# Performance work log

Measured on AMD Instinct MI355X. Metric: run time of the kernel, lower is better.

The kernel has to match this reference:

```python
import jax, jax.numpy as jnp
import numpy as np
import math

N = 8_000_000
EPS = 0.0


def setup_inputs() -> dict:
    key = jax.random.key(0)
    x = jax.random.normal(key, (N, 3), dtype=jnp.float32)
    return {"x": x}


def _normalize(x, eps):
    # faithful to _safe_norm: sn = sum(x^2) + eps^2; eps==0 -> guard zero vectors
    sn = jnp.sum(x * x, axis=-1, keepdims=True) + eps * eps
    if eps == 0.0:
        sn_safe = jnp.where(sn == 0.0, 1.0, sn)
        inv = jnp.where(sn == 0.0, 0.0, jax.lax.rsqrt(sn_safe))
        return x * inv
    return x * jax.lax.rsqrt(sn)


def _sh_l0to3(u):
    # u: (..., 3) unit vectors; real spherical harmonics, e3nn/cuEquivariance
    # "component" normalization (|Y^l(u)|^2 = 2l+1 on the unit sphere).
    vx, vy, vz = u[..., 0], u[..., 1], u[..., 2]
    x2, y2, z2 = vx * vx, vy * vy, vz * vz
    x2z2 = x2 + z2

    sh0 = jnp.ones_like(vx)[..., None]                      # (..., 1)

    sh1 = math.sqrt(3.0) * u                                # (..., 3)

    s15 = math.sqrt(15.0)
    sh2_0 = s15 * vx * vz
    sh2_1 = s15 * vx * vy
    sh2_2 = math.sqrt(5.0) * (y2 - 0.5 * x2z2)
    sh2_3 = s15 * vy * vz
    sh2_4 = 0.5 * s15 * (z2 - x2)
    sh2 = jnp.stack([sh2_0, sh2_1, sh2_2, sh2_3, sh2_4], axis=-1)  # (..., 5)

    c42_6 = math.sqrt(42.0) / 6.0
    c168_8 = math.sqrt(168.0) / 8.0
    s7 = math.sqrt(7.0)
    sh3_0 = c42_6 * (sh2_0 * vz + sh2_4 * vx)
    sh3_1 = s7 * sh2_0 * vy
    sh3_2 = c168_8 * (4.0 * y2 - x2z2) * vx
    sh3_3 = 0.5 * s7 * vy * (2.0 * y2 - 3.0 * x2z2)
    sh3_4 = c168_8 * vz * (4.0 * y2 - x2z2)
    sh3_5 = s7 * sh2_4 * vy
    sh3_6 = c42_6 * (sh2_4 * vz - sh2_0 * vx)
    sh3 = jnp.stack([sh3_0, sh3_1, sh3_2, sh3_3, sh3_4, sh3_5, sh3_6], axis=-1)  # (..., 7)

    return sh0, sh1, sh2, sh3


def reference(x):
    shape = x.shape[:-1]
    u = _normalize(x, EPS)
    outs = _sh_l0to3(u)
    # original returns {ir: y.reshape(shape + (1, ir.dim))} for l = 0..max_degree
    return tuple(y.reshape(shape + (1, y.shape[-1])) for y in outs)
```

## Files before the change

### kernel.cpp

```cpp
#include <hip/hip_runtime.h>
#include <math.h>


__device__ __forceinline__ void compute_sh(float px, float py, float pz,
                                           float* __restrict__ s1,
                                           float* __restrict__ s2,
                                           float* __restrict__ s3) {
    float sn = px * px + py * py + pz * pz;
    float inv = (sn == 0.0f) ? 0.0f : rsqrtf(sn);
    float vx = px * inv, vy = py * inv, vz = pz * inv;

    const float SQ3 = 1.7320508075688772f;
    const float S15 = 3.872983346207417f;
    const float SQ5 = 2.23606797749979f;
    const float C42_6 = 1.0801234497346435f;
    const float C168_8 = 1.6201851746019651f;
    const float S7 = 2.6457513110645907f;

    float x2 = vx * vx, y2 = vy * vy, z2 = vz * vz;
    float x2z2 = x2 + z2;

    s1[0] = SQ3 * vx;
    s1[1] = SQ3 * vy;
    s1[2] = SQ3 * vz;

    float sh2_0 = S15 * vx * vz;
    float sh2_4 = 0.5f * S15 * (z2 - x2);
    s2[0] = sh2_0;
    s2[1] = S15 * vx * vy;
    s2[2] = SQ5 * (y2 - 0.5f * x2z2);
    s2[3] = S15 * vy * vz;
    s2[4] = sh2_4;

    float q = 4.0f * y2 - x2z2;
    s3[0] = C42_6 * (sh2_0 * vz + sh2_4 * vx);
    s3[1] = S7 * sh2_0 * vy;
    s3[2] = C168_8 * q * vx;
    s3[3] = 0.5f * S7 * vy * (2.0f * y2 - 3.0f * x2z2);
    s3[4] = C168_8 * vz * q;
    s3[5] = S7 * sh2_4 * vy;
    s3[6] = C42_6 * (sh2_4 * vz - sh2_0 * vx);
}

__global__ __launch_bounds__(256) void sh_kernel(const float* __restrict__ x,
                                                 float* __restrict__ out,
                                                 long long nvec) {
    long long nvec4 = nvec >> 2;
    long long rem = nvec & 3;
    long long t = (long long)blockIdx.x * blockDim.x + threadIdx.x;

    float* out0 = out;
    float* out1 = out + nvec;
    float* out2 = out + 4 * nvec;
    float* out3 = out + 9 * nvec;

    if (t < nvec4) {
        const float4* xp = (const float4*)x;
        float in[12];
        float4 a = xp[3 * t + 0];
        float4 b = xp[3 * t + 1];
        float4 c = xp[3 * t + 2];
        in[0] = a.x; in[1] = a.y; in[2]  = a.z; in[3]  = a.w;
        in[4] = b.x; in[5] = b.y; in[6]  = b.z; in[7]  = b.w;
        in[8] = c.x; in[9] = c.y; in[10] = c.z; in[11] = c.w;

        float o1[12], o2[20], o3[28];
#pragma unroll
        for (int k = 0; k < 4; ++k) {
            compute_sh(in[3 * k], in[3 * k + 1], in[3 * k + 2],
                       &o1[3 * k], &o2[5 * k], &o3[7 * k]);
        }

        ((float4*)out0)[t] = make_float4(1.0f, 1.0f, 1.0f, 1.0f);
        float4* p1 = (float4*)(out1 + 12 * t);
#pragma unroll
        for (int k = 0; k < 3; ++k)
            p1[k] = make_float4(o1[4 * k], o1[4 * k + 1], o1[4 * k + 2], o1[4 * k + 3]);
        float4* p2 = (float4*)(out2 + 20 * t);
#pragma unroll
        for (int k = 0; k < 5; ++k)
            p2[k] = make_float4(o2[4 * k], o2[4 * k + 1], o2[4 * k + 2], o2[4 * k + 3]);
        float4* p3 = (float4*)(out3 + 28 * t);
#pragma unroll
        for (int k = 0; k < 7; ++k)
            p3[k] = make_float4(o3[4 * k], o3[4 * k + 1], o3[4 * k + 2], o3[4 * k + 3]);
    } else if (t == nvec4 && rem) {
        for (long long i = nvec4 * 4; i < nvec; ++i) {
            float s1[3], s2[5], s3[7];
            compute_sh(x[3 * i], x[3 * i + 1], x[3 * i + 2], s1, s2, s3);
            out0[i] = 1.0f;
            for (int k = 0; k < 3; ++k) out1[3 * i + k] = s1[k];
            for (int k = 0; k < 5; ++k) out2[5 * i + k] = s2[k];
            for (int k = 0; k < 7; ++k) out3[7 * i + k] = s3[k];
        }
    }
}

extern "C" void kernel_launch(void* const* d_in, const int* in_sizes, int n_in,
                              void* d_out, int out_size, void* d_ws, size_t ws_size,
                              hipStream_t stream) {
    const float* x = (const float*)d_in[0];
    float* out = (float*)d_out;
    long long nvec = (long long)in_sizes[0] / 3;
    long long threads_needed = (nvec >> 2) + ((nvec & 3) ? 1 : 0);
    int block = 256;
    long long grid = (threads_needed + block - 1) / block;
    sh_kernel<<<(dim3)(unsigned)grid, block, 0, stream>>>(x, out, nvec);
}
```

Baseline: 616.2 us.

## Stage SH outputs through LDS for coalesced nontemporal global stores

```diff
diff --git a/kernel.cpp b/kernel.cpp
--- a/kernel.cpp
+++ b/kernel.cpp
@@ -1,6 +1,11 @@
 #include <hip/hip_runtime.h>
 #include <math.h>
 
+
+typedef float f32x4 __attribute__((ext_vector_type(4)));
+
+#define BLOCK 256
+#define VPB   512
 
 __device__ __forceinline__ void compute_sh(float px, float py, float pz,
                                            float* __restrict__ s1,
@@ -42,50 +47,76 @@
     s3[6] = C42_6 * (sh2_4 * vz - sh2_0 * vx);
 }
 
-__global__ __launch_bounds__(256) void sh_kernel(const float* __restrict__ x,
-                                                 float* __restrict__ out,
-                                                 long long nvec) {
-    long long nvec4 = nvec >> 2;
-    long long rem = nvec & 3;
-    long long t = (long long)blockIdx.x * blockDim.x + threadIdx.x;
+__global__ __launch_bounds__(BLOCK) void sh_kernel(const float* __restrict__ x,
+                                                   float* __restrict__ out,
+                                                   long long nvec) {
+    __shared__ float lds[15 * VPB];
+    float* lds1 = lds;
+    float* lds2 = lds + 3 * VPB;
+    float* lds3 = lds + 8 * VPB;
+
+    const int lt = threadIdx.x;
+    const long long base = (long long)blockIdx.x * VPB;
 
     float* out0 = out;
     float* out1 = out + nvec;
     float* out2 = out + 4 * nvec;
     float* out3 = out + 9 * nvec;
 
-    if (t < nvec4) {
-        const float4* xp = (const float4*)x;
-        float in[12];
-        float4 a = xp[3 * t + 0];
-        float4 b = xp[3 * t + 1];
-        float4 c = xp[3 * t + 2];
-        in[0] = a.x; in[1] = a.y; in[2]  = a.z; in[3]  = a.w;
-        in[4] = b.x; in[5] = b.y; in[6]  = b.z; in[7]  = b.w;
-        in[8] = c.x; in[9] = c.y; in[10] = c.z; in[11] = c.w;
+    long long cnt = nvec - base;
 
-        float o1[12], o2[20], o3[28];
+    if (cnt >= VPB) {
+        const float* xin = x + 3 * base;
 #pragma unroll
-        for (int k = 0; k < 4; ++k) {
-            compute_sh(in[3 * k], in[3 * k + 1], in[3 * k + 2],
-                       &o1[3 * k], &o2[5 * k], &o3[7 * k]);
+        for (int k = 0; k < 2; ++k) {
+            const int v = lt + BLOCK * k;
+            float s1[3], s2[5], s3[7];
+            compute_sh(xin[3 * v + 0], xin[3 * v + 1], xin[3 * v + 2],
+                       s1, s2, s3);
+#pragma unroll
+            for (int c = 0; c < 3; ++c) lds1[3 * v + c] = s1[c];
+#pragma unroll
+            for (int c = 0; c < 5; ++c) lds2[5 * v + c] = s2[c];
+#pragma unroll
+            for (int c = 0; c < 7; ++c) lds3[7 * v + c] = s3[c];
+        }
+        __syncthreads();
+
+        if (lt < VPB / 4) {
+            f32x4 ones = {1.0f, 1.0f, 1.0f, 1.0f};
+            __builtin_nontemporal_store(ones, (f32x4*)(out0 + base) + lt);
         }
 
-        ((float4*)out0)[t] = make_float4(1.0f, 1.0f, 1.0f, 1.0f);
-        float4* p1 = (float4*)(out1 + 12 * t);
+        if ((nvec & 3) == 0) {
+            const f32x4* l1 = (const f32x4*)lds1;
+            const f32x4* l2 = (const f32x4*)lds2;
+            const f32x4* l3 = (const f32x4*)lds3;
+            f32x4* g1 = (f32x4*)(out1 + 3 * base);
+            f32x4* g2 = (f32x4*)(out2 + 5 * base);
+            f32x4* g3 = (f32x4*)(out3 + 7 * base);
+
+            __builtin_nontemporal_store(l1[lt], g1 + lt);
+            if (lt < 128)
+                __builtin_nontemporal_store(l1[256 + lt], g1 + 256 + lt);
+
 #pragma unroll
-        for (int k = 0; k < 3; ++k)
-            p1[k] = make_float4(o1[4 * k], o1[4 * k + 1], o1[4 * k + 2], o1[4 * k + 3]);
-        float4* p2 = (float4*)(out2 + 20 * t);
+            for (int k = 0; k < 2; ++k)
+                __builtin_nontemporal_store(l2[k * 256 + lt], g2 + k * 256 + lt);
+            if (lt < 128)
+                __builtin_nontemporal_store(l2[512 + lt], g2 + 512 + lt);
+
 #pragma unroll
-        for (int k = 0; k < 5; ++k)
-            p2[k] = make_float4(o2[4 * k], o2[4 * k + 1], o2[4 * k + 2], o2[4 * k + 3]);
-        float4* p3 = (float4*)(out3 + 28 * t);
-#pragma unroll
-        for (int k = 0; k < 7; ++k)
-            p3[k] = make_float4(o3[4 * k], o3[4 * k + 1], o3[4 * k + 2], o3[4 * k + 3]);
-    } else if (t == nvec4 && rem) {
-        for (long long i = nvec4 * 4; i < nvec; ++i) {
+            for (int k = 0; k < 3; ++k)
+                __builtin_nontemporal_store(l3[k * 256 + lt], g3 + k * 256 + lt);
+            if (lt < 128)
+                __builtin_nontemporal_store(l3[768 + lt], g3 + 768 + lt);
+        } else {
+            for (int i = lt; i < 3 * VPB; i += BLOCK) out1[3 * base + i] = lds1[i];
+            for (int i = lt; i < 5 * VPB; i += BLOCK) out2[5 * base + i] = lds2[i];
+            for (int i = lt; i < 7 * VPB; i += BLOCK) out3[7 * base + i] = lds3[i];
+        }
+    } else {
+        for (long long i = base + lt; i < nvec; i += BLOCK) {
             float s1[3], s2[5], s3[7];
             compute_sh(x[3 * i], x[3 * i + 1], x[3 * i + 2], s1, s2, s3);
             out0[i] = 1.0f;
@@ -102,8 +133,6 @@
     const float* x = (const float*)d_in[0];
     float* out = (float*)d_out;
     long long nvec = (long long)in_sizes[0] / 3;
-    long long threads_needed = (nvec >> 2) + ((nvec & 3) ? 1 : 0);
-    int block = 256;
-    long long grid = (threads_needed + block - 1) / block;
-    sh_kernel<<<(dim3)(unsigned)grid, block, 0, stream>>>(x, out, nvec);
+    long long grid = (nvec + VPB - 1) / VPB;
+    sh_kernel<<<dim3((unsigned)grid), BLOCK, 0, stream>>>(x, out, nvec);
 }
```

Measured after the change: 558.7 us. 1.1x faster.
